# Kernel tuning notes

Measured on AMD Instinct MI355X. Metric: run time of the kernel, lower is better.

Reference implementation:

```python
import jax, jax.numpy as jnp
import numpy as np

B, C_IN, H, W = 1024, 3, 32, 32
D_IN = C_IN * H * W          # 3072, matches input_size
R_HID = 128                  # router hidden_size
E = 8                        # num experts
TOP_K = 2
E_HID = 2048                 # expert MLP hidden
N_CLS = 10                   # cifar classes


def setup_inputs() -> dict:
    key = jax.random.key(0)
    ks = jax.random.split(key, 10)
    s = lambda fan_in: 1.0 / np.sqrt(fan_in)
    x = jax.random.normal(ks[0], (B, C_IN, H, W), jnp.float32)
    # router params
    rW1 = jax.random.normal(ks[1], (D_IN, R_HID), jnp.float32) * s(D_IN)
    rb1 = jnp.zeros((R_HID,), jnp.float32)
    rW2 = jax.random.normal(ks[2], (R_HID, E), jnp.float32) * s(R_HID)
    rb2 = jnp.zeros((E,), jnp.float32)
    # stacked expert params [E, ...]
    eW1 = jax.random.normal(ks[3], (E, D_IN, E_HID), jnp.float32) * s(D_IN)
    eb1 = jnp.zeros((E, E_HID), jnp.float32)
    eW2 = jax.random.normal(ks[4], (E, E_HID, N_CLS), jnp.float32) * s(E_HID)
    eb2 = jnp.zeros((E, N_CLS), jnp.float32)
    return {"x": x, "rW1": rW1, "rb1": rb1, "rW2": rW2, "rb2": rb2,
            "eW1": eW1, "eb1": eb1, "eW2": eW2, "eb2": eb2}


def reference(x, rW1, rb1, rW2, rb2, eW1, eb1, eW2, eb2):
    b = x.shape[0]
    xf = x.reshape(b, -1)                                  # [B, D_IN]
    # router (eval mode: no noise, no dropout)
    rh = jax.nn.relu(xf @ rW1 + rb1)
    logits = rh @ rW2 + rb2                                # [B, E]
    rw = jax.nn.softmax(logits, axis=-1)
    w, idx = jax.lax.top_k(rw, TOP_K)                      # [B, K]
    w = w / jnp.sum(w, axis=-1, keepdims=True)
    # dense per-expert compute (same math as masked dispatch)
    eh = jax.nn.relu(jnp.einsum('bd,edh->ebh', xf, eW1) + eb1[:, None, :])  # [E,B,H]
    outs = jnp.einsum('ebh,ehc->ebc', eh, eW2) + eb2[:, None, :]            # [E,B,C]
    # combine: gather each sample's top-k expert outputs
    taken = outs[idx.T, jnp.arange(b)[None, :]]            # [K, B, C]
    return jnp.sum(w.T[:, :, None] * taken, axis=0)        # [B, C]
```

## Files before the change

### kernel.cpp

```cpp
#include <hip/hip_runtime.h>
#include <cstdint>
#include <cstddef>

#define B_TOK 1024
#define DD_IN 3072
#define RHID 128
#define NEXP 8
#define EHID 2048
#define NCLS 10

typedef __attribute__((ext_vector_type(8))) short short8;
typedef __attribute__((ext_vector_type(4))) float floatx4;

__device__ __forceinline__ unsigned short f2bf(float f) {
  unsigned u = __builtin_bit_cast(unsigned, f);
  u += 0x7fffu + ((u >> 16) & 1u);
  return (unsigned short)(u >> 16);
}
__device__ __forceinline__ unsigned pk_bf16(float a, float b) {
  return (unsigned)f2bf(a) | ((unsigned)f2bf(b) << 16);
}
__device__ __forceinline__ float bf2f(unsigned short h) {
  unsigned u = ((unsigned)h) << 16;
  return __builtin_bit_cast(float, u);
}

__global__ __launch_bounds__(256) void k_router_gemm(const float* __restrict__ x,
                                                     const float* __restrict__ rW1,
                                                     float* __restrict__ partial) {
  const int ttile = blockIdx.x;
  const int s = blockIdx.y;
  const int T0 = ttile * 64;
  const int K0 = s * 192;
  __shared__ float xs[16][64];
  __shared__ float wsm[16][132];
  float acc[4][8];
#pragma unroll
  for (int i = 0; i < 4; i++)
#pragma unroll
    for (int j = 0; j < 8; j++) acc[i][j] = 0.f;
  const int tx = threadIdx.x & 15, ty = threadIdx.x >> 4;
  const int tid = threadIdx.x;

  const int xtok = tid >> 2, xk = (tid & 3) << 2;
  const int wk0 = tid >> 5, wf0 = (tid & 31) << 2;

  float4 pX, pW0, pW1;
  pX  = *(const float4*)(x + (size_t)(T0 + xtok) * DD_IN + K0 + xk);
  pW0 = *(const float4*)(rW1 + (size_t)(K0 + wk0) * RHID + wf0);
  pW1 = *(const float4*)(rW1 + (size_t)(K0 + wk0 + 8) * RHID + wf0);

  for (int kc = K0; kc < K0 + 192; kc += 16) {
    xs[xk + 0][xtok] = pX.x; xs[xk + 1][xtok] = pX.y;
    xs[xk + 2][xtok] = pX.z; xs[xk + 3][xtok] = pX.w;
    *(float4*)&wsm[wk0][wf0] = pW0;
    *(float4*)&wsm[wk0 + 8][wf0] = pW1;
    __syncthreads();
    if (kc + 16 < K0 + 192) {
      pX  = *(const float4*)(x + (size_t)(T0 + xtok) * DD_IN + kc + 16 + xk);
      pW0 = *(const float4*)(rW1 + (size_t)(kc + 16 + wk0) * RHID + wf0);
      pW1 = *(const float4*)(rW1 + (size_t)(kc + 16 + wk0 + 8) * RHID + wf0);
    }
#pragma unroll
    for (int kk = 0; kk < 16; kk++) {
      float wv[8], xv[4];
      *(float4*)&wv[0] = *(const float4*)&wsm[kk][tx * 8];
      *(float4*)&wv[4] = *(const float4*)&wsm[kk][tx * 8 + 4];
#pragma unroll
      for (int i = 0; i < 4; i++) xv[i] = xs[kk][ty * 4 + i];
#pragma unroll
      for (int i = 0; i < 4; i++)
#pragma unroll
        for (int j = 0; j < 8; j++) acc[i][j] += xv[i] * wv[j];
    }
    __syncthreads();
  }
#pragma unroll
  for (int i = 0; i < 4; i++) {
    float* p = partial + ((size_t)s * B_TOK + T0 + ty * 4 + i) * RHID + tx * 8;
    *(float4*)p = *(float4*)&acc[i][0];
    *(float4*)(p + 4) = *(float4*)&acc[i][4];
  }
}

__global__ __launch_bounds__(256) void k_router_fin(const float* __restrict__ partial,
                                                    const float* __restrict__ rb1,
                                                    const float* __restrict__ rW2,
                                                    const float* __restrict__ rb2,
                                                    const float* __restrict__ eb2,
                                                    float* __restrict__ out,
                                                    int* __restrict__ cnt,
                                                    int* __restrict__ tokL,
                                                    float* __restrict__ wtL) {
  if (threadIdx.x < 4 * NCLS)
    out[blockIdx.x * 4 * NCLS + threadIdx.x] = eb2[threadIdx.x % NCLS];
  const int lane = threadIdx.x & 63;
  const int tok = blockIdx.x * 4 + (threadIdx.x >> 6);
  float r0 = 0.f, r1 = 0.f;
#pragma unroll
  for (int s = 0; s < 16; s++) {
    const float* p = partial + ((size_t)s * B_TOK + tok) * RHID;
    r0 += p[lane]; r1 += p[lane + 64];
  }
  r0 = fmaxf(r0 + rb1[lane], 0.f);
  r1 = fmaxf(r1 + rb1[lane + 64], 0.f);
  float lg[8];
#pragma unroll
  for (int c = 0; c < 8; c++)
    lg[c] = r0 * rW2[lane * 8 + c] + r1 * rW2[(lane + 64) * 8 + c];
#pragma unroll
  for (int off = 32; off >= 1; off >>= 1)
#pragma unroll
    for (int c = 0; c < 8; c++) lg[c] += __shfl_down(lg[c], off);
  if (lane == 0) {
    float m1 = -1e30f, m2 = -1e30f; int i1 = 0, i2 = 0;
#pragma unroll
    for (int c = 0; c < 8; c++) {
      float l = lg[c] + rb2[c];
      if (l > m1) { m2 = m1; i2 = i1; m1 = l; i1 = c; }
      else if (l > m2) { m2 = l; i2 = c; }
    }
    float w1 = 1.f / (1.f + expf(m2 - m1));
    float w2 = 1.f - w1;
    int p1 = atomicAdd(&cnt[i1], 1);
    tokL[i1 * B_TOK + p1] = tok; wtL[i1 * B_TOK + p1] = w1;
    int p2 = atomicAdd(&cnt[i2], 1);
    tokL[i2 * B_TOK + p2] = tok; wtL[i2 * B_TOK + p2] = w2;
  }
}

__global__ __launch_bounds__(256, 2) void k_expert(const float* __restrict__ x,
                                                   const float* __restrict__ eW1,
                                                   const float* __restrict__ eb1,
                                                   const float* __restrict__ eW2,
                                                   const int* __restrict__ cnt,
                                                   const int* __restrict__ tokL,
                                                   const float* __restrict__ wtL,
                                                   float* __restrict__ out) {
  const int nt = blockIdx.x;
  int mt = blockIdx.y;
  int e = 0;
#pragma unroll
  for (e = 0; e < NEXP; e++) {
    int te = (cnt[e] + 127) >> 7;
    if (mt < te) break;
    mt -= te;
  }
  if (e >= NEXP) return;
  const int cnt_e = cnt[e];

  __shared__ union {
    struct { unsigned short As[128][72]; unsigned Bs[32][132]; } a;
    struct { unsigned short ehs[128][132]; float w2[128 * NCLS]; } b;
  } u;
  __shared__ int stok[128];
  __shared__ float swt[128];

  const int tid = threadIdx.x;
  if (tid < 128) {
    int r = mt * 128 + tid;
    bool v = r < cnt_e;
    stok[tid] = v ? tokL[e * B_TOK + r] : -1;
    swt[tid]  = v ? wtL[e * B_TOK + r] : 0.f;
  }
  __syncthreads();

  const int lane = tid & 63;
  const int wv = tid >> 6;
  const int wm = (wv & 1) * 64, wn = (wv >> 1) * 64;
  const int col = lane & 15, quad = lane >> 4;

  floatx4 acc[4][4];
#pragma unroll
  for (int mi = 0; mi < 4; mi++)
#pragma unroll
    for (int ni = 0; ni < 4; ni++) acc[mi][ni] = (floatx4)0.f;

  const float* W1e = eW1 + (size_t)e * DD_IN * EHID + (size_t)nt * 128;

  const int arow = tid >> 4, ac4 = (tid & 15) << 2;
  const int bk2 = tid >> 5, bn4 = (tid & 31) << 2;

  float4 pA[8];
  float4 pBa[4], pBb[4];

#pragma unroll
  for (int i = 0; i < 8; i++) {
    int tk = stok[arow + i * 16];
    pA[i] = (tk >= 0) ? *(const float4*)(x + (size_t)tk * DD_IN + ac4)
                      : make_float4(0.f, 0.f, 0.f, 0.f);
  }
#pragma unroll
  for (int i = 0; i < 4; i++) {
    const float* src = W1e + (size_t)((bk2 + i * 8) * 2) * EHID + bn4;
    pBa[i] = *(const float4*)src;
    pBb[i] = *(const float4*)(src + EHID);
  }

  for (int k0 = 0; k0 < DD_IN; k0 += 64) {
#pragma unroll
    for (int i = 0; i < 8; i++) {
      uint2 w;
      w.x = pk_bf16(pA[i].x, pA[i].y);
      w.y = pk_bf16(pA[i].z, pA[i].w);
      *(uint2*)&u.a.As[arow + i * 16][ac4] = w;
    }
#pragma unroll
    for (int i = 0; i < 4; i++) {
      uint4 w;
      w.x = pk_bf16(pBa[i].x, pBb[i].x); w.y = pk_bf16(pBa[i].y, pBb[i].y);
      w.z = pk_bf16(pBa[i].z, pBb[i].z); w.w = pk_bf16(pBa[i].w, pBb[i].w);
      *(uint4*)&u.a.Bs[bk2 + i * 8][bn4] = w;
    }
    __syncthreads();
    if (k0 + 64 < DD_IN) {
#pragma unroll
      for (int i = 0; i < 8; i++) {
        int tk = stok[arow + i * 16];
        pA[i] = (tk >= 0) ? *(const float4*)(x + (size_t)tk * DD_IN + k0 + 64 + ac4)
                          : make_float4(0.f, 0.f, 0.f, 0.f);
      }
#pragma unroll
      for (int i = 0; i < 4; i++) {
        const float* src = W1e + (size_t)(k0 + 64 + (bk2 + i * 8) * 2) * EHID + bn4;
        pBa[i] = *(const float4*)src;
        pBb[i] = *(const float4*)(src + EHID);
      }
    }
#pragma unroll
    for (int kk = 0; kk < 2; kk++) {
      short8 af[4], bf[4];
#pragma unroll
      for (int mi = 0; mi < 4; mi++)
        af[mi] = *(const short8*)&u.a.As[wm + mi * 16 + col][kk * 32 + quad * 8];
#pragma unroll
      for (int ni = 0; ni < 4; ni++) {
        int kb = kk * 16 + quad * 4;
        int nb = wn + ni * 16 + col;
        uint4 t;
        t.x = u.a.Bs[kb + 0][nb]; t.y = u.a.Bs[kb + 1][nb];
        t.z = u.a.Bs[kb + 2][nb]; t.w = u.a.Bs[kb + 3][nb];
        bf[ni] = __builtin_bit_cast(short8, t);
      }
#pragma unroll
      for (int mi = 0; mi < 4; mi++)
#pragma unroll
        for (int ni = 0; ni < 4; ni++)
          acc[mi][ni] = __builtin_amdgcn_mfma_f32_16x16x32_bf16(af[mi], bf[ni], acc[mi][ni], 0, 0, 0);
    }
    __syncthreads();
  }
#pragma unroll
  for (int ni = 0; ni < 4; ni++) {
    int hid = wn + ni * 16 + col;
    float bias = eb1[(size_t)e * EHID + nt * 128 + hid];
#pragma unroll
    for (int mi = 0; mi < 4; mi++)
#pragma unroll
      for (int r = 0; r < 4; r++) {
        float val = fmaxf(acc[mi][ni][r] + bias, 0.f);
        u.b.ehs[wm + mi * 16 + quad * 4 + r][hid] = f2bf(val);
      }
  }
#pragma unroll
  for (int i = 0; i < 5; i++) {
    int idx = tid + i * 256;
    if (idx < 128 * NCLS)
      u.b.w2[idx] = eW2[((size_t)e * EHID + nt * 128 + idx / NCLS) * NCLS + (idx % NCLS)];
  }
  __syncthreads();
  {
    int tok = tid >> 1, half = tid & 1;
    float a10[NCLS];
#pragma unroll
    for (int c = 0; c < NCLS; c++) a10[c] = 0.f;
    for (int hh = 0; hh < 64; hh++) {
      int h = half * 64 + hh;
      float eh = bf2f(u.b.ehs[tok][h]);
#pragma unroll
      for (int c = 0; c < NCLS; c++) a10[c] += eh * u.b.w2[h * NCLS + c];
    }
    int tk = stok[tok];
    if (tk >= 0) {
      float wt = swt[tok];
#pragma unroll
      for (int c = 0; c < NCLS; c++)
        atomicAdd(out + (size_t)tk * NCLS + c, wt * a10[c]);
    }
  }
}

extern "C" void kernel_launch(void* const* d_in, const int* in_sizes, int n_in,
                              void* d_out, int out_size, void* d_ws, size_t ws_size,
                              hipStream_t stream) {
  const float* x   = (const float*)d_in[0];
  const float* rW1 = (const float*)d_in[1];
  const float* rb1 = (const float*)d_in[2];
  const float* rW2 = (const float*)d_in[3];
  const float* rb2 = (const float*)d_in[4];
  const float* eW1 = (const float*)d_in[5];
  const float* eb1 = (const float*)d_in[6];
  const float* eW2 = (const float*)d_in[7];
  const float* eb2 = (const float*)d_in[8];
  float* out = (float*)d_out;

  char* ws = (char*)d_ws;
  int*   cnt     = (int*)(ws + 0);
  int*   tokL    = (int*)(ws + 1024);
  float* wtL     = (float*)(ws + 33792);
  float* partial = (float*)(ws + 66560);

  hipMemsetAsync(cnt, 0, 1024, stream);
  k_router_gemm<<<dim3(16, 16), 256, 0, stream>>>(x, rW1, partial);
  k_router_fin<<<256, 256, 0, stream>>>(partial, rb1, rW2, rb2, eb2, out, cnt, tokL, wtL);
  k_expert<<<dim3(16, 23), 256, 0, stream>>>(x, eW1, eb1, eW2, cnt, tokL, wtL, out);
}
```

Baseline: 437.5 us.

## Pre-convert x to bf16 in router and pipeline expert GEMM with async LDS loads

The router GEMM now also writes a bf16 copy of x and zeroes the expert counters, which removes the separate memset. The expert kernel moves to 256-token tiles with 512 threads. It loads A straight from the bf16 buffer into LDS through global_load_lds, using a swizzled layout and double buffering. B loads are software-pipelined with explicit waitcnt and barriers, so gather and convert overhead overlap the MFMA work. The cost is extra workspace, heavier LDS and register use, and larger tiles that may pad more rows per expert.

```diff
diff --git a/kernel.cpp b/kernel.cpp
--- a/kernel.cpp
+++ b/kernel.cpp
@@ -24,10 +24,17 @@
   unsigned u = ((unsigned)h) << 16;
   return __builtin_bit_cast(float, u);
 }
+__device__ __forceinline__ void gload16(const void* g, void* l) {
+  __builtin_amdgcn_global_load_lds((const __attribute__((address_space(1))) void*)g,
+                                   (__attribute__((address_space(3))) void*)l, 16, 0, 0);
+}
 
 __global__ __launch_bounds__(256) void k_router_gemm(const float* __restrict__ x,
                                                      const float* __restrict__ rW1,
-                                                     float* __restrict__ partial) {
+                                                     float* __restrict__ partial,
+                                                     unsigned short* __restrict__ xbf,
+                                                     int* __restrict__ cnt) {
+  if (blockIdx.x == 0 && blockIdx.y == 0 && threadIdx.x < NEXP) cnt[threadIdx.x] = 0;
   const int ttile = blockIdx.x;
   const int s = blockIdx.y;
   const int T0 = ttile * 64;
@@ -53,6 +60,12 @@
   for (int kc = K0; kc < K0 + 192; kc += 16) {
     xs[xk + 0][xtok] = pX.x; xs[xk + 1][xtok] = pX.y;
     xs[xk + 2][xtok] = pX.z; xs[xk + 3][xtok] = pX.w;
+    {
+      uint2 xw;
+      xw.x = pk_bf16(pX.x, pX.y);
+      xw.y = pk_bf16(pX.z, pX.w);
+      *(uint2*)(xbf + (size_t)(T0 + xtok) * DD_IN + kc + xk) = xw;
+    }
     *(float4*)&wsm[wk0][wf0] = pW0;
     *(float4*)&wsm[wk0 + 8][wf0] = pW1;
     __syncthreads();
@@ -129,7 +142,55 @@
   }
 }
 
-__global__ __launch_bounds__(256, 2) void k_expert(const float* __restrict__ x,
+#define ISSUE_B(s_) do { _Pragma("unroll") for (int i_ = 0; i_ < 2; i_++) { \
+    sBa[s_][i_] = *(const float4*)pB[i_]; \
+    sBb[s_][i_] = *(const float4*)(pB[i_] + EHID); \
+    pB[i_] += (size_t)64 * EHID; } } while (0)
+
+#define ISSUE_A(p_) do { _Pragma("unroll") for (int i_ = 0; i_ < 4; i_++) { \
+    gload16((const void*)srcA[i_], (void*)&u.a.As[p_][i_ * 64 + w8][0]); \
+    srcA[i_] += 64; } } while (0)
+
+#define CONV_B(s_) do { _Pragma("unroll") for (int i_ = 0; i_ < 2; i_++) { \
+    uint4 wv_; \
+    wv_.x = pk_bf16(sBa[s_][i_].x, sBb[s_][i_].x); \
+    wv_.y = pk_bf16(sBa[s_][i_].y, sBb[s_][i_].y); \
+    wv_.z = pk_bf16(sBa[s_][i_].z, sBb[s_][i_].z); \
+    wv_.w = pk_bf16(sBa[s_][i_].w, sBb[s_][i_].w); \
+    *(uint4*)&u.a.Bs[bk + i_ * 16][bn4] = wv_; } } while (0)
+
+#define PIPE_SYNC(N_) do { \
+    asm volatile("s_waitcnt vmcnt(" #N_ ") lgkmcnt(0)" ::: "memory"); \
+    __builtin_amdgcn_sched_barrier(0); \
+    __builtin_amdgcn_s_barrier(); \
+    __builtin_amdgcn_sched_barrier(0); } while (0)
+
+#define END_BAR do { \
+    __builtin_amdgcn_sched_barrier(0); \
+    __builtin_amdgcn_s_barrier(); \
+    __builtin_amdgcn_sched_barrier(0); } while (0)
+
+#define MFMA_PH(p_) do { \
+  _Pragma("unroll") for (int kk = 0; kk < 2; kk++) { \
+    short8 af[4], bfr[4]; \
+    _Pragma("unroll") for (int mi = 0; mi < 4; mi++) { \
+      int row_ = wm + mi * 16 + col; \
+      int cs_ = (kk * 4 + quad) ^ (row_ & 7); \
+      af[mi] = *(const short8*)((const char*)&u.a.As[p_][0][0] + row_ * 128 + (cs_ << 4)); \
+    } \
+    _Pragma("unroll") for (int ni = 0; ni < 4; ni++) { \
+      int kb_ = kk * 16 + quad * 4, nb_ = wn + ni * 16 + col; \
+      uint4 t_; \
+      t_.x = u.a.Bs[kb_ + 0][nb_]; t_.y = u.a.Bs[kb_ + 1][nb_]; \
+      t_.z = u.a.Bs[kb_ + 2][nb_]; t_.w = u.a.Bs[kb_ + 3][nb_]; \
+      bfr[ni] = __builtin_bit_cast(short8, t_); \
+    } \
+    _Pragma("unroll") for (int mi = 0; mi < 4; mi++) \
+      _Pragma("unroll") for (int ni = 0; ni < 4; ni++) \
+        acc[mi][ni] = __builtin_amdgcn_mfma_f32_16x16x32_bf16(af[mi], bfr[ni], acc[mi][ni], 0, 0, 0); \
+  } } while (0)
+
+__global__ __launch_bounds__(512, 2) void k_expert(const unsigned short* __restrict__ xbf,
                                                    const float* __restrict__ eW1,
                                                    const float* __restrict__ eb1,
                                                    const float* __restrict__ eW2,
@@ -142,7 +203,7 @@
   int e = 0;
 #pragma unroll
   for (e = 0; e < NEXP; e++) {
-    int te = (cnt[e] + 127) >> 7;
+    int te = (cnt[e] + 255) >> 8;
     if (mt < te) break;
     mt -= te;
   }
@@ -150,15 +211,15 @@
   const int cnt_e = cnt[e];
 
   __shared__ union {
-    struct { unsigned short As[128][72]; unsigned Bs[32][132]; } a;
-    struct { unsigned short ehs[128][132]; float w2[128 * NCLS]; } b;
+    struct { unsigned short As[2][256][64]; unsigned Bs[32][132]; } a;
+    struct { unsigned short ehs[256][132]; float w2[128 * NCLS]; } b;
   } u;
-  __shared__ int stok[128];
-  __shared__ float swt[128];
+  __shared__ int stok[256];
+  __shared__ float swt[256];
 
   const int tid = threadIdx.x;
-  if (tid < 128) {
-    int r = mt * 128 + tid;
+  if (tid < 256) {
+    int r = mt * 256 + tid;
     bool v = r < cnt_e;
     stok[tid] = v ? tokL[e * B_TOK + r] : -1;
     swt[tid]  = v ? wtL[e * B_TOK + r] : 0.f;
@@ -167,7 +228,8 @@
 
   const int lane = tid & 63;
   const int wv = tid >> 6;
-  const int wm = (wv & 1) * 64, wn = (wv >> 1) * 64;
+  const int w8 = wv << 3;
+  const int wm = (wv >> 1) * 64, wn = (wv & 1) * 64;
   const int col = lane & 15, quad = lane >> 4;
 
   floatx4 acc[4][4];
@@ -176,80 +238,44 @@
 #pragma unroll
     for (int ni = 0; ni < 4; ni++) acc[mi][ni] = (floatx4)0.f;
 
+  const int r8 = tid >> 3, c16 = tid & 7;
+  const int c16s = c16 ^ (r8 & 7);
+  const unsigned short* srcA[4];
+#pragma unroll
+  for (int i = 0; i < 4; i++) {
+    int tk = stok[r8 + i * 64];
+    if (tk < 0) tk = 0;
+    srcA[i] = xbf + (size_t)tk * DD_IN + (c16s << 3);
+  }
   const float* W1e = eW1 + (size_t)e * DD_IN * EHID + (size_t)nt * 128;
-
-  const int arow = tid >> 4, ac4 = (tid & 15) << 2;
-  const int bk2 = tid >> 5, bn4 = (tid & 31) << 2;
-
-  float4 pA[8];
-  float4 pBa[4], pBb[4];
-
-#pragma unroll
-  for (int i = 0; i < 8; i++) {
-    int tk = stok[arow + i * 16];
-    pA[i] = (tk >= 0) ? *(const float4*)(x + (size_t)tk * DD_IN + ac4)
-                      : make_float4(0.f, 0.f, 0.f, 0.f);
-  }
-#pragma unroll
-  for (int i = 0; i < 4; i++) {
-    const float* src = W1e + (size_t)((bk2 + i * 8) * 2) * EHID + bn4;
-    pBa[i] = *(const float4*)src;
-    pBb[i] = *(const float4*)(src + EHID);
-  }
-
-  for (int k0 = 0; k0 < DD_IN; k0 += 64) {
-#pragma unroll
-    for (int i = 0; i < 8; i++) {
-      uint2 w;
-      w.x = pk_bf16(pA[i].x, pA[i].y);
-      w.y = pk_bf16(pA[i].z, pA[i].w);
-      *(uint2*)&u.a.As[arow + i * 16][ac4] = w;
-    }
-#pragma unroll
-    for (int i = 0; i < 4; i++) {
-      uint4 w;
-      w.x = pk_bf16(pBa[i].x, pBb[i].x); w.y = pk_bf16(pBa[i].y, pBb[i].y);
-      w.z = pk_bf16(pBa[i].z, pBb[i].z); w.w = pk_bf16(pBa[i].w, pBb[i].w);
-      *(uint4*)&u.a.Bs[bk2 + i * 8][bn4] = w;
-    }
-    __syncthreads();
-    if (k0 + 64 < DD_IN) {
-#pragma unroll
-      for (int i = 0; i < 8; i++) {
-        int tk = stok[arow + i * 16];
-        pA[i] = (tk >= 0) ? *(const float4*)(x + (size_t)tk * DD_IN + k0 + 64 + ac4)
-                          : make_float4(0.f, 0.f, 0.f, 0.f);
-      }
-#pragma unroll
-      for (int i = 0; i < 4; i++) {
-        const float* src = W1e + (size_t)(k0 + 64 + (bk2 + i * 8) * 2) * EHID + bn4;
-        pBa[i] = *(const float4*)src;
-        pBb[i] = *(const float4*)(src + EHID);
-      }
-    }
-#pragma unroll
-    for (int kk = 0; kk < 2; kk++) {
-      short8 af[4], bf[4];
-#pragma unroll
-      for (int mi = 0; mi < 4; mi++)
-        af[mi] = *(const short8*)&u.a.As[wm + mi * 16 + col][kk * 32 + quad * 8];
-#pragma unroll
-      for (int ni = 0; ni < 4; ni++) {
-        int kb = kk * 16 + quad * 4;
-        int nb = wn + ni * 16 + col;
-        uint4 t;
-        t.x = u.a.Bs[kb + 0][nb]; t.y = u.a.Bs[kb + 1][nb];
-        t.z = u.a.Bs[kb + 2][nb]; t.w = u.a.Bs[kb + 3][nb];
-        bf[ni] = __builtin_bit_cast(short8, t);
-      }
-#pragma unroll
-      for (int mi = 0; mi < 4; mi++)
-#pragma unroll
-        for (int ni = 0; ni < 4; ni++)
-          acc[mi][ni] = __builtin_amdgcn_mfma_f32_16x16x32_bf16(af[mi], bf[ni], acc[mi][ni], 0, 0, 0);
-    }
-    __syncthreads();
-  }
+  const int bk = tid >> 5, bn4 = (tid & 31) << 2;
+  const float* pB[2];
+#pragma unroll
+  for (int i = 0; i < 2; i++) pB[i] = W1e + (size_t)(2 * (bk + i * 16)) * EHID + bn4;
+
+  float4 sBa[2][2], sBb[2][2];
+
+  ISSUE_B(0);
+  ISSUE_A(0);
+
+  for (int t = 0; t < 48; t += 2) {
+    ISSUE_B(1); ISSUE_A(1);
+    CONV_B(0);
+    PIPE_SYNC(8);
+    MFMA_PH(0);
+    END_BAR;
+    if (t < 46) {
+      ISSUE_B(0); ISSUE_A(0);
+      CONV_B(1);
+      PIPE_SYNC(8);
+    } else {
+      CONV_B(1);
+      PIPE_SYNC(0);
+    }
+    MFMA_PH(1);
+    END_BAR;
+  }
+
 #pragma unroll
   for (int ni = 0; ni < 4; ni++) {
     int hid = wn + ni * 16 + col;
@@ -263,8 +289,8 @@
       }
   }
 #pragma unroll
-  for (int i = 0; i < 5; i++) {
-    int idx = tid + i * 256;
+  for (int i = 0; i < 3; i++) {
+    int idx = tid + i * 512;
     if (idx < 128 * NCLS)
       u.b.w2[idx] = eW2[((size_t)e * EHID + nt * 128 + idx / NCLS) * NCLS + (idx % NCLS)];
   }
@@ -309,9 +335,9 @@
   int*   tokL    = (int*)(ws + 1024);
   float* wtL     = (float*)(ws + 33792);
   float* partial = (float*)(ws + 66560);
-
-  hipMemsetAsync(cnt, 0, 1024, stream);
-  k_router_gemm<<<dim3(16, 16), 256, 0, stream>>>(x, rW1, partial);
+  unsigned short* xbf = (unsigned short*)(ws + 66560 + (size_t)16 * B_TOK * RHID * 4);
+
+  k_router_gemm<<<dim3(16, 16), 256, 0, stream>>>(x, rW1, partial, xbf, cnt);
   k_router_fin<<<256, 256, 0, stream>>>(partial, rb1, rW2, rb2, eb2, out, cnt, tokL, wtL);
-  k_expert<<<dim3(16, 23), 256, 0, stream>>>(x, eW1, eb1, eW2, cnt, tokL, wtL, out);
-}
+  k_expert<<<dim3(16, 16), 512, 0, stream>>>(xbf, eW1, eb1, eW2, cnt, tokL, wtL, out);
+}
```

New measurement: 455.6 us. 1.04x slower.
